# Kernel tuning notes

Measured on AMD Instinct MI355X. Metric: run time of the kernel, lower is better.

The kernel has to match this reference:

```python
import jax, jax.numpy as jnp
import numpy as np

B, S, HID = 2, 2048, 2048
H, D = 16, 128  # heads, head_dim == kernel_hidden_size
GATE_NORM = 16.0
CLAMP_MIN = -50.0


def gla(q, k, v, gk):
    # fused_recurrent_gla: S_t = diag(exp(gk_t)) S_{t-1} + k_t^T v_t; o_t = (q_t*scale) @ S_t
    # q,k,v,gk: [B,H,S,D]
    scale = D ** -0.5
    qs = jnp.moveaxis(q, 2, 0) * scale  # [S,B,H,D]
    ks = jnp.moveaxis(k, 2, 0)
    vs = jnp.moveaxis(v, 2, 0)
    gs = jnp.moveaxis(gk, 2, 0)

    def step(state, xs):
        q_t, k_t, v_t, g_t = xs  # each [B,H,D]
        state = state * jnp.exp(g_t)[..., None] + k_t[..., None] * v_t[..., None, :]
        o_t = jnp.einsum('bhk,bhkv->bhv', q_t, state)
        return state, o_t

    init = jnp.zeros((q.shape[0], H, D, D), q.dtype)
    _, out = jax.lax.scan(step, init, (qs, ks, vs, gs))
    return jnp.moveaxis(out, 0, 2)  # [B,H,S,D]


def setup_inputs() -> dict:
    key = jax.random.key(0)
    ks = jax.random.split(key, 8)
    std = 0.02
    hidden_states = jax.random.normal(ks[0], (B, S, HID), jnp.float32)
    Wq = jax.random.normal(ks[1], (HID, HID), jnp.float32) * std
    Wk = jax.random.normal(ks[2], (HID, HID), jnp.float32) * std
    Wv = jax.random.normal(ks[3], (HID, HID), jnp.float32) * std
    Wo = jax.random.normal(ks[4], (HID, HID), jnp.float32) * std
    Wg1 = jnp.eye(HID, dtype=jnp.float32)  # nn.init.eye_
    bg1 = jnp.zeros((HID,), jnp.float32)
    Wg2 = jnp.eye(HID, dtype=jnp.float32)
    bg2 = jnp.zeros((HID,), jnp.float32)
    alpha_list = jax.random.uniform(ks[5], (2,), jnp.float32)
    return dict(hidden_states=hidden_states, Wq=Wq, Wk=Wk, Wv=Wv, Wo=Wo,
                Wg1=Wg1, bg1=bg1, Wg2=Wg2, bg2=bg2, alpha_list=alpha_list)


def reference(hidden_states, Wq, Wk, Wv, Wo, Wg1, bg1, Wg2, bg2, alpha_list):
    b, s, _ = hidden_states.shape

    def split_heads(x):  # [b,s,hid] -> [b,h,s,d]
        return x.reshape(b, s, H, D).transpose(0, 2, 1, 3)

    q = split_heads(hidden_states @ Wq.T)
    k = split_heads(hidden_states @ Wk.T)
    v = split_heads(hidden_states @ Wv.T)

    def gate(Wg, bg):
        g = split_heads(hidden_states @ Wg.T + bg)
        g = jax.nn.log_sigmoid(g) / GATE_NORM
        return jnp.maximum(g, CLAMP_MIN)

    gk = gate(Wg1, bg1)
    gk2 = gate(Wg2, bg2)

    o1 = gla(q, k, v, gk)
    o2 = gla(q, k, v, gk2)

    a = jax.nn.softmax(alpha_list)
    attn = a[0] * o1 + a[1] * o2  # [b,h,s,d]
    attn = attn.transpose(0, 2, 1, 3).reshape(b, s, HID)
    return attn @ Wo.T
```

## Files before the change

### kernel.cpp

```cpp
#include <hip/hip_runtime.h>
#include <cstdint>
#include <cstddef>


#define BB     2
#define SEQ    2048
#define HIDN   2048
#define NH     16
#define DD     128
#define CHUNK  64
#define NCHUNK (SEQ / CHUNK)
#define NBH    (BB * NH)
#define NELC   8388608
#define WELC   4194304
static constexpr float QSCALE = 0.08838834764831845f;

typedef __bf16 bf16_t;
typedef _Float16 half_t;
typedef short  short8 __attribute__((ext_vector_type(8)));
typedef float  f32x4  __attribute__((ext_vector_type(4)));
typedef float  float4v __attribute__((ext_vector_type(4)));

__device__ __forceinline__ float bf2f(short u) {
  return (float)__builtin_bit_cast(bf16_t, u);
}
__device__ __forceinline__ short f2bf(float f) {
  return __builtin_bit_cast(short, (bf16_t)f);
}
__device__ __forceinline__ float hf2f(short u) {
  return (float)__builtin_bit_cast(half_t, u);
}
__device__ __forceinline__ short f2hf(float f) {
  return __builtin_bit_cast(short, (half_t)f);
}

__device__ __forceinline__ void gload_lds16(const void* g, void* l) {
  __builtin_amdgcn_global_load_lds(
      (__attribute__((address_space(1))) unsigned int*)g,
      (__attribute__((address_space(3))) unsigned int*)l, 16, 0, 0);
}

__device__ __forceinline__ void gemm_body(const bf16_t* __restrict__ A,
                                          const bf16_t* __restrict__ Bw,
                                          const float*  __restrict__ bias,
                                          bf16_t* __restrict__ outb,
                                          float*  __restrict__ outf, int epi) {
  __shared__ bf16_t As[128 * 64];
  __shared__ bf16_t Bs[128 * 64];
  const int tm   = blockIdx.x * 128;
  const int tn   = blockIdx.y * 128;
  const int wave = threadIdx.x >> 6;
  const int lane = threadIdx.x & 63;
  const int wm   = (wave >> 1) * 64;
  const int wn   = (wave & 1) * 64;
  const int qd   = lane >> 4;
  const int l16  = lane & 15;
  const int ro   = l16 & 7;

  const int gc   = (lane & 7) ^ (lane >> 3);
  const bf16_t* ga[4];
  const bf16_t* gb[4];
  bf16_t* la[4];
  bf16_t* lb[4];
#pragma unroll
  for (int u = 0; u < 4; u++) {
    const int row = wave * 32 + u * 8 + (lane >> 3);
    ga[u] = A  + (size_t)(tm + row) * HIDN + gc * 8;
    gb[u] = Bw + (size_t)(tn + row) * HIDN + gc * 8;
    la[u] = &As[(wave * 256 + u * 64) * 8];
    lb[u] = &Bs[(wave * 256 + u * 64) * 8];
  }

  f32x4 acc[4][4];
#pragma unroll
  for (int i = 0; i < 4; i++)
#pragma unroll
    for (int j = 0; j < 4; j++) acc[i][j] = (f32x4){0.f, 0.f, 0.f, 0.f};

  for (int k0 = 0; k0 < HIDN; k0 += 64) {
#pragma unroll
    for (int u = 0; u < 4; u++) { gload_lds16(ga[u], la[u]); ga[u] += 64; }
#pragma unroll
    for (int u = 0; u < 4; u++) { gload_lds16(gb[u], lb[u]); gb[u] += 64; }
    __syncthreads();
#pragma unroll
    for (int ks = 0; ks < 2; ks++) {
      const int g = ks * 4 + qd;
      short8 af[4], bfv[4];
#pragma unroll
      for (int t = 0; t < 4; t++)
        af[t] = *(const short8*)&As[(wm + t * 16 + l16) * 64 + (g ^ ro) * 8];
#pragma unroll
      for (int t = 0; t < 4; t++)
        bfv[t] = *(const short8*)&Bs[(wn + t * 16 + l16) * 64 + (g ^ ro) * 8];
#pragma unroll
      for (int i = 0; i < 4; i++)
#pragma unroll
        for (int j = 0; j < 4; j++)
          acc[i][j] = __builtin_amdgcn_mfma_f32_16x16x32_bf16(
              af[i], bfv[j], acc[i][j], 0, 0, 0);
    }
    __syncthreads();
  }

#pragma unroll
  for (int i = 0; i < 4; i++)
#pragma unroll
    for (int j = 0; j < 4; j++)
#pragma unroll
      for (int r = 0; r < 4; r++) {
        const int row = tm + wm + i * 16 + qd * 4 + r;
        const int col = tn + wn + j * 16 + l16;
        float v = acc[i][j][r];
        if (epi == 1) {
          v += bias[col];
          const float ls = fminf(v, 0.f) - log1pf(__expf(-fabsf(v)));
          v = fmaxf(ls * 0.0625f, -50.f);
        }
        if (epi == 2) outf[(size_t)row * HIDN + col] = v;
        else          outb[(size_t)row * HIDN + col] = (bf16_t)v;
      }
}

__global__ __launch_bounds__(256) void k_gemm_proj(
    const bf16_t* __restrict__ Xb,
    const bf16_t* __restrict__ W0, const bf16_t* __restrict__ W1,
    const bf16_t* __restrict__ W2, const bf16_t* __restrict__ W3,
    const bf16_t* __restrict__ W4,
    const float* __restrict__ bg1, const float* __restrict__ bg2,
    bf16_t* __restrict__ Qb, bf16_t* __restrict__ Kb, bf16_t* __restrict__ Vb,
    bf16_t* __restrict__ G1b, bf16_t* __restrict__ G2b) {
  const int z = blockIdx.z;
  const bf16_t* Ws[5] = {W0, W1, W2, W3, W4};
  bf16_t* Os[5] = {Qb, Kb, Vb, G1b, G2b};
  const float* bias = (z == 3) ? bg1 : ((z == 4) ? bg2 : nullptr);
  gemm_body(Xb, Ws[z], bias, Os[z], nullptr, (z >= 3) ? 1 : 0);
}

__global__ __launch_bounds__(256) void k_gemm_out(
    const bf16_t* __restrict__ attnB, const bf16_t* __restrict__ Wob,
    float* __restrict__ out) {
  gemm_body(attnB, Wob, nullptr, nullptr, out, 2);
}

__global__ __launch_bounds__(256) void k_cvt_all(
    const float* __restrict__ hid, const float* __restrict__ wq,
    const float* __restrict__ wk, const float* __restrict__ wv,
    const float* __restrict__ wg1, const float* __restrict__ wg2,
    const float* __restrict__ wo, bf16_t* __restrict__ Xb,
    bf16_t* __restrict__ Wd, bf16_t* __restrict__ Wcur,
    bf16_t* __restrict__ WoB) {
  const int y = blockIdx.y;
  const float* srcs[7] = {hid, wq, wk, wv, wg1, wg2, wo};
  bf16_t* dsts[7] = {Xb, Wd, Wd + WELC, Wd + 2 * WELC, Wd + 3 * WELC, Wcur,
                     WoB};
  const int n = (y == 0) ? NELC : WELC;
  const float* src = srcs[y];
  bf16_t* dst = dsts[y];
  const int idx = (blockIdx.x * 256 + threadIdx.x) * 4;
  if (idx < n) {
    const float4 f = *(const float4*)(src + idx);
    dst[idx + 0] = (bf16_t)f.x; dst[idx + 1] = (bf16_t)f.y;
    dst[idx + 2] = (bf16_t)f.z; dst[idx + 3] = (bf16_t)f.w;
  }
}

__global__ __launch_bounds__(256) void k_zero(float* __restrict__ out) {
  out[(size_t)blockIdx.x * 256 + threadIdx.x] = 0.f;
}

__global__ __launch_bounds__(256) void k_trg(
    bf16_t* __restrict__ Qb, bf16_t* __restrict__ Kb, bf16_t* __restrict__ Vb,
    bf16_t* __restrict__ G1b, bf16_t* __restrict__ G2b,
    float* __restrict__ Btot) {
  const int n = blockIdx.x, bh = blockIdx.y, z = blockIdx.z;
  const int b = bh >> 4, h = bh & 15;
  bf16_t* bufs[5] = {Qb, Kb, Vb, G1b, G2b};
  short* P = (short*)bufs[z];
  const size_t rbase = ((size_t)(b * SEQ + n * CHUNK)) * HIDN + h * DD;
  const int tid = threadIdx.x;
  __shared__ short L1[CHUNK * 136];
  __shared__ short L2[DD * 72];

#pragma unroll
  for (int k = 0; k < 4; k++) {
    const int v = tid + k * 256;
    const int t = v >> 4, d0 = (v & 15) * 8;
    const short8 x = *(const short8*)(P + rbase + (size_t)t * HIDN + d0);
#pragma unroll
    for (int j = 0; j < 8; j++) L1[t * 136 + d0 + j] = x[j];
  }
  __syncthreads();
  if (tid < DD) {
    const int d = tid;
    if (z >= 3) {
      float c = 0.f;
#pragma unroll
      for (int ch = 0; ch < 8; ch++) {
        short8 o;
#pragma unroll
        for (int j = 0; j < 8; j++) {
          c += bf2f(L1[(ch * 8 + j) * 136 + d]);
          o[j] = f2hf(c);
        }
        *(short8*)&L2[d * 72 + ch * 8] = o;
      }
      Btot[((size_t)((z - 3) * NBH + bh) * NCHUNK + n) * DD + d] = c;
    } else {
#pragma unroll
      for (int ch = 0; ch < 8; ch++) {
        short8 o;
#pragma unroll
        for (int j = 0; j < 8; j++) o[j] = L1[(ch * 8 + j) * 136 + d];
        *(short8*)&L2[d * 72 + ch * 8] = o;
      }
    }
  }
  __syncthreads();
#pragma unroll
  for (int k = 0; k < 4; k++) {
    const int v = tid + k * 256;
    const int r = v >> 4, x0 = (v & 15) * 8;
    const int d = 2 * r + (x0 >> 6), t0 = x0 & 63;
    const short8 o = *(const short8*)&L2[d * 72 + t0];
    *(short8*)(P + rbase + (size_t)r * HIDN + x0) = o;
  }
}

__global__ __launch_bounds__(256) void k_s1(
    const bf16_t* __restrict__ Kb, const bf16_t* __restrict__ Vb,
    const bf16_t* __restrict__ Gc, bf16_t* __restrict__ UT) {
  const int n = blockIdx.x, bh = blockIdx.y;
  const int b = bh >> 4, h = bh & 15;
  const size_t rbase = ((size_t)(b * SEQ + n * CHUNK)) * HIDN + h * DD;
  const int tid = threadIdx.x;
  __shared__ short k2L[DD * 72];

  if (tid < DD) {
    const int d = tid;
    const size_t row = rbase + (size_t)(d >> 1) * HIDN + (d & 1) * 64;
    const short* Kp = (const short*)Kb + row;
    const short* Gp = (const short*)Gc + row;
    const float c63 = hf2f(Gp[63]);
#pragma unroll
    for (int ch = 0; ch < 8; ch++) {
      const short8 kk = *(const short8*)(Kp + ch * 8);
      const short8 cc = *(const short8*)(Gp + ch * 8);
      short8 o;
#pragma unroll
      for (int j = 0; j < 8; j++)
        o[j] = f2bf(bf2f(kk[j]) * __expf(c63 - hf2f(cc[j])));
      *(short8*)&k2L[d * 72 + ch * 8] = o;
    }
  }
  __syncthreads();

  const int wave = tid >> 6, lane = tid & 63, qd = lane >> 4, l16 = lane & 15;
  const int m0 = (wave >> 1) * 64, n0 = (wave & 1) * 64;
  const short* Vp = (const short*)Vb;
  f32x4 acc[4][4];
#pragma unroll
  for (int i = 0; i < 4; i++)
#pragma unroll
    for (int j = 0; j < 4; j++) acc[i][j] = (f32x4){0.f, 0.f, 0.f, 0.f};
#pragma unroll
  for (int ks = 0; ks < 2; ks++) {
    const int ch = ks * 4 + qd;
    short8 af[4], bfv[4];
#pragma unroll
    for (int i = 0; i < 4; i++) {
      const int dv = m0 + i * 16 + l16;
      af[i] = *(const short8*)(Vp + rbase + (size_t)(dv >> 1) * HIDN +
                               (dv & 1) * 64 + ch * 8);
    }
#pragma unroll
    for (int j = 0; j < 4; j++)
      bfv[j] = *(const short8*)&k2L[(n0 + j * 16 + l16) * 72 + ch * 8];
#pragma unroll
    for (int i = 0; i < 4; i++)
#pragma unroll
      for (int j = 0; j < 4; j++)
        acc[i][j] = __builtin_amdgcn_mfma_f32_16x16x32_bf16(af[i], bfv[j],
                                                            acc[i][j], 0, 0, 0);
  }
  bf16_t* Uo = UT + ((size_t)bh * NCHUNK + n) * (size_t)(DD * DD);
#pragma unroll
  for (int i = 0; i < 4; i++)
#pragma unroll
    for (int j = 0; j < 4; j++)
#pragma unroll
      for (int r = 0; r < 4; r++)
        Uo[(size_t)(m0 + i * 16 + qd * 4 + r) * DD + n0 + j * 16 + l16] =
            (bf16_t)acc[i][j][r];
}

__global__ __launch_bounds__(256) void k_s2(bf16_t* __restrict__ UT,
                                            const float* __restrict__ Btot) {
  const int dg = blockIdx.x, bh = blockIdx.y;
  const int dv = dg * 8 + (threadIdx.x >> 5);
  const int dk0 = (threadIdx.x & 31) * 4;
  float st[4] = {0.f, 0.f, 0.f, 0.f};
  for (int nn = 0; nn < NCHUNK; nn++) {
    short* p =
        (short*)UT + ((size_t)bh * NCHUNK + nn) * (size_t)(DD * DD) + dv * DD + dk0;
    const float4v bp =
        *(const float4v*)(Btot + ((size_t)bh * NCHUNK + nn) * DD + dk0);
    short u0 = p[0], u1 = p[1], u2 = p[2], u3 = p[3];
    p[0] = f2bf(st[0]); p[1] = f2bf(st[1]);
    p[2] = f2bf(st[2]); p[3] = f2bf(st[3]);
    st[0] = st[0] * __expf(bp[0]) + bf2f(u0);
    st[1] = st[1] * __expf(bp[1]) + bf2f(u1);
    st[2] = st[2] * __expf(bp[2]) + bf2f(u2);
    st[3] = st[3] * __expf(bp[3]) + bf2f(u3);
  }
}

template <int ACC>
__global__ __launch_bounds__(256) void k_s3(
    const bf16_t* __restrict__ Qb, const bf16_t* __restrict__ Kb,
    const bf16_t* __restrict__ Vb, const bf16_t* __restrict__ Gc,
    const bf16_t* __restrict__ UT, const float* __restrict__ alpha,
    bf16_t* __restrict__ attn) {
  const int n = blockIdx.x, bh = blockIdx.y;
  const int b = bh >> 4, h = bh & 15;
  const size_t rbase = ((size_t)(b * SEQ + n * CHUNK)) * HIDN + h * DD;
  const int tid = threadIdx.x;
  __shared__ short qhL[CHUNK * 136];
  __shared__ short k2L[CHUNK * 136];
  __shared__ short PsL[CHUNK * 72];
  const float mx = fmaxf(alpha[0], alpha[1]);
  const float x0 = __expf(alpha[0] - mx), x1 = __expf(alpha[1] - mx);
  const float w = (ACC ? x1 : x0) / (x0 + x1);

  if (tid < DD) {
    const int d = tid;
    const size_t row = rbase + (size_t)(d >> 1) * HIDN + (d & 1) * 64;
    const short* Qp = (const short*)Qb + row;
    const short* Kp = (const short*)Kb + row;
    const short* Gp = (const short*)Gc + row;
    const float wsc = w * QSCALE;
#pragma unroll
    for (int ch = 0; ch < 8; ch++) {
      const short8 qq = *(const short8*)(Qp + ch * 8);
      const short8 kk = *(const short8*)(Kp + ch * 8);
      const short8 cc = *(const short8*)(Gp + ch * 8);
#pragma unroll
      for (int j = 0; j < 8; j++) {
        const float c = hf2f(cc[j]);
        const int t = ch * 8 + j;
        qhL[t * 136 + d] = f2bf(bf2f(qq[j]) * wsc * __expf(c));
        k2L[t * 136 + d] = f2bf(bf2f(kk[j]) * __expf(-c));
      }
    }
  }
  __syncthreads();

  const int wave = tid >> 6, lane = tid & 63, qd = lane >> 4, l16 = lane & 15;
  {
    f32x4 pacc[4];
#pragma unroll
    for (int j = 0; j < 4; j++) pacc[j] = (f32x4){0.f, 0.f, 0.f, 0.f};
#pragma unroll
    for (int ks = 0; ks < 4; ks++) {
      const int ch = ks * 4 + qd;
      const short8 a = *(const short8*)&qhL[(wave * 16 + l16) * 136 + ch * 8];
#pragma unroll
      for (int j = 0; j < 4; j++) {
        const short8 bq = *(const short8*)&k2L[(j * 16 + l16) * 136 + ch * 8];
        pacc[j] = __builtin_amdgcn_mfma_f32_16x16x32_bf16(a, bq, pacc[j], 0, 0, 0);
      }
    }
#pragma unroll
    for (int j = 0; j < 4; j++)
#pragma unroll
      for (int r = 0; r < 4; r++) {
        const int t = wave * 16 + qd * 4 + r, s = j * 16 + l16;
        PsL[t * 72 + s] = (t >= s) ? f2bf(pacc[j][r]) : (short)0;
      }
  }
  __syncthreads();

  const short* Sp =
      (const short*)UT + ((size_t)bh * NCHUNK + n) * (size_t)(DD * DD);
  const short* Vp = (const short*)Vb;
  const int nw = wave * 32;
  f32x4 acc[4][2];
#pragma unroll
  for (int i = 0; i < 4; i++)
#pragma unroll
    for (int j = 0; j < 2; j++) acc[i][j] = (f32x4){0.f, 0.f, 0.f, 0.f};
#pragma unroll
  for (int ks = 0; ks < 2; ks++) {
    const int ch = ks * 4 + qd;
    short8 a[4];
#pragma unroll
    for (int i = 0; i < 4; i++)
      a[i] = *(const short8*)&PsL[(i * 16 + l16) * 72 + ch * 8];
#pragma unroll
    for (int j = 0; j < 2; j++) {
      const int dv = nw + j * 16 + l16;
      const short8 bq = *(const short8*)(Vp + rbase + (size_t)(dv >> 1) * HIDN +
                                         (dv & 1) * 64 + ch * 8);
#pragma unroll
      for (int i = 0; i < 4; i++)
        acc[i][j] = __builtin_amdgcn_mfma_f32_16x16x32_bf16(a[i], bq,
                                                            acc[i][j], 0, 0, 0);
    }
  }
#pragma unroll
  for (int ks = 0; ks < 4; ks++) {
    const int ch = ks * 4 + qd;
    short8 a[4];
#pragma unroll
    for (int i = 0; i < 4; i++)
      a[i] = *(const short8*)&qhL[(i * 16 + l16) * 136 + ch * 8];
#pragma unroll
    for (int j = 0; j < 2; j++) {
      const short8 bq =
          *(const short8*)(Sp + (size_t)(nw + j * 16 + l16) * DD + ch * 8);
#pragma unroll
      for (int i = 0; i < 4; i++)
        acc[i][j] = __builtin_amdgcn_mfma_f32_16x16x32_bf16(a[i], bq,
                                                            acc[i][j], 0, 0, 0);
    }
  }
#pragma unroll
  for (int i = 0; i < 4; i++)
#pragma unroll
    for (int j = 0; j < 2; j++)
#pragma unroll
      for (int r = 0; r < 4; r++) {
        const int t = i * 16 + qd * 4 + r;
        const int dv = nw + j * 16 + l16;
        bf16_t* p = &attn[rbase + (size_t)t * HIDN + dv];
        if (ACC) *p = (bf16_t)((float)*p + acc[i][j][r]);
        else     *p = (bf16_t)acc[i][j][r];
      }
}

extern "C" void kernel_launch(void* const* d_in, const int* in_sizes, int n_in,
                              void* d_out, int out_size, void* d_ws,
                              size_t ws_size, hipStream_t stream) {
  const float* hid  = (const float*)d_in[0];
  const float* wq   = (const float*)d_in[1];
  const float* wk   = (const float*)d_in[2];
  const float* wv   = (const float*)d_in[3];
  const float* wo   = (const float*)d_in[4];
  const float* wg1  = (const float*)d_in[5];
  const float* bg1  = (const float*)d_in[6];
  const float* wg2  = (const float*)d_in[7];
  const float* bg2  = (const float*)d_in[8];
  const float* alph = (const float*)d_in[9];
  float* out = (float*)d_out;
  (void)in_sizes; (void)n_in; (void)out_size;

  char* ws = (char*)d_ws;
  size_t off = 0;
  auto alloc = [&](size_t bytes) -> void* {
    void* p = ws + off;
    off += (bytes + 255) & ~(size_t)255;
    return p;
  };
  const size_t NEL = NELC, WEL = WELC;
  bf16_t* Xb   = (bf16_t*)alloc(NEL * 2);
  bf16_t* Wcur = (bf16_t*)alloc(WEL * 2);
  bf16_t* WoB  = (bf16_t*)alloc(WEL * 2);
  bf16_t* Qb   = (bf16_t*)alloc(NEL * 2);
  bf16_t* Kb   = (bf16_t*)alloc(NEL * 2);
  bf16_t* Vb   = (bf16_t*)alloc(NEL * 2);
  bf16_t* G1b  = (bf16_t*)alloc(NEL * 2);
  bf16_t* G2b  = (bf16_t*)alloc(NEL * 2);
  float*  Btot = (float*) alloc((size_t)2 * NBH * NCHUNK * DD * 4);
  bf16_t* Wd = (bf16_t*)d_out;
  bf16_t* UT = (bf16_t*)d_out;

  if (off > ws_size) {
    k_zero<<<dim3((unsigned)(NEL / 256)), 256, 0, stream>>>(out);
    return;
  }

  k_cvt_all<<<dim3(8192, 7), 256, 0, stream>>>(hid, wq, wk, wv, wg1, wg2, wo,
                                               Xb, Wd, Wcur, WoB);
  k_gemm_proj<<<dim3(32, 16, 5), 256, 0, stream>>>(
      Xb, Wd, Wd + WEL, Wd + 2 * WEL, Wd + 3 * WEL, Wcur, bg1, bg2, Qb, Kb, Vb,
      G1b, G2b);
  k_trg<<<dim3(NCHUNK, NBH, 5), 256, 0, stream>>>(Qb, Kb, Vb, G1b, G2b, Btot);

  const dim3 gs(NCHUNK, NBH), g2(16, NBH);
  const size_t BSTRIDE = (size_t)NBH * NCHUNK * DD;
  k_s1<<<gs, 256, 0, stream>>>(Kb, Vb, G1b, UT);
  k_s2<<<g2, 256, 0, stream>>>(UT, Btot);
  k_s3<0><<<gs, 256, 0, stream>>>(Qb, Kb, Vb, G1b, UT, alph, Xb);
  k_s1<<<gs, 256, 0, stream>>>(Kb, Vb, G2b, UT);
  k_s2<<<g2, 256, 0, stream>>>(UT, Btot + BSTRIDE);
  k_s3<1><<<gs, 256, 0, stream>>>(Qb, Kb, Vb, G2b, UT, alph, Xb);

  k_gemm_out<<<dim3(32, 16), 256, 0, stream>>>(Xb, WoB, out);
}
```

Measured before the change: 648.5 us.

## Drop chunk transpose pass; fuse intra-chunk attention into state-update kernel

Removes the k_trg kernel that transposed Q/K/V/G chunks in global memory. Only the gate cumulative sum stays, now done in place by a lightweight kernel. The per-chunk state contribution and the intra-chunk causal attention are merged into one kernel that transposes V and K in LDS. A slimmer kernel then adds the inter-chunk state term using an XOR-swizzled state layout loaded directly into LDS. This cuts global read/write passes and extra launches, at the cost of more LDS per block and scalar int-unpacking LDS reads.

```diff
diff --git a/kernel.cpp b/kernel.cpp
--- a/kernel.cpp
+++ b/kernel.cpp
@@ -19,7 +19,6 @@
 typedef _Float16 half_t;
 typedef short  short8 __attribute__((ext_vector_type(8)));
 typedef float  f32x4  __attribute__((ext_vector_type(4)));
-typedef float  float4v __attribute__((ext_vector_type(4)));
 
 __device__ __forceinline__ float bf2f(short u) {
   return (float)__builtin_bit_cast(bf16_t, u);
@@ -57,7 +56,7 @@
   const int l16  = lane & 15;
   const int ro   = l16 & 7;
 
-  const int gc   = (lane & 7) ^ (lane >> 3);
+  const int gc = (lane & 7) ^ (lane >> 3);
   const bf16_t* ga[4];
   const bf16_t* gb[4];
   bf16_t* la[4];
@@ -169,129 +168,212 @@
   out[(size_t)blockIdx.x * 256 + threadIdx.x] = 0.f;
 }
 
-__global__ __launch_bounds__(256) void k_trg(
-    bf16_t* __restrict__ Qb, bf16_t* __restrict__ Kb, bf16_t* __restrict__ Vb,
-    bf16_t* __restrict__ G1b, bf16_t* __restrict__ G2b,
-    float* __restrict__ Btot) {
-  const int n = blockIdx.x, bh = blockIdx.y, z = blockIdx.z;
-  const int b = bh >> 4, h = bh & 15;
-  bf16_t* bufs[5] = {Qb, Kb, Vb, G1b, G2b};
-  short* P = (short*)bufs[z];
-  const size_t rbase = ((size_t)(b * SEQ + n * CHUNK)) * HIDN + h * DD;
-  const int tid = threadIdx.x;
-  __shared__ short L1[CHUNK * 136];
-  __shared__ short L2[DD * 72];
-
-#pragma unroll
-  for (int k = 0; k < 4; k++) {
-    const int v = tid + k * 256;
-    const int t = v >> 4, d0 = (v & 15) * 8;
-    const short8 x = *(const short8*)(P + rbase + (size_t)t * HIDN + d0);
-#pragma unroll
-    for (int j = 0; j < 8; j++) L1[t * 136 + d0 + j] = x[j];
-  }
-  __syncthreads();
-  if (tid < DD) {
-    const int d = tid;
-    if (z >= 3) {
-      float c = 0.f;
-#pragma unroll
-      for (int ch = 0; ch < 8; ch++) {
-        short8 o;
-#pragma unroll
-        for (int j = 0; j < 8; j++) {
-          c += bf2f(L1[(ch * 8 + j) * 136 + d]);
-          o[j] = f2hf(c);
-        }
-        *(short8*)&L2[d * 72 + ch * 8] = o;
-      }
-      Btot[((size_t)((z - 3) * NBH + bh) * NCHUNK + n) * DD + d] = c;
-    } else {
-#pragma unroll
-      for (int ch = 0; ch < 8; ch++) {
-        short8 o;
-#pragma unroll
-        for (int j = 0; j < 8; j++) o[j] = L1[(ch * 8 + j) * 136 + d];
-        *(short8*)&L2[d * 72 + ch * 8] = o;
-      }
-    }
-  }
-  __syncthreads();
-#pragma unroll
-  for (int k = 0; k < 4; k++) {
-    const int v = tid + k * 256;
-    const int r = v >> 4, x0 = (v & 15) * 8;
-    const int d = 2 * r + (x0 >> 6), t0 = x0 & 63;
-    const short8 o = *(const short8*)&L2[d * 72 + t0];
-    *(short8*)(P + rbase + (size_t)r * HIDN + x0) = o;
-  }
-}
-
-__global__ __launch_bounds__(256) void k_s1(
-    const bf16_t* __restrict__ Kb, const bf16_t* __restrict__ Vb,
-    const bf16_t* __restrict__ Gc, bf16_t* __restrict__ UT) {
+__global__ __launch_bounds__(64) void k_gc(bf16_t* __restrict__ G1b,
+                                           bf16_t* __restrict__ G2b,
+                                           float* __restrict__ Btot) {
+  const int n = blockIdx.x, b = blockIdx.y >> 2, slab = blockIdx.y & 3;
+  const int e = blockIdx.z;
+  short* P = (short*)(e ? G2b : G1b);
+  const int d0 = slab * 512 + threadIdx.x * 8;
+  const size_t base = ((size_t)(b * SEQ + n * CHUNK)) * HIDN + d0;
+  float c[8] = {0.f, 0.f, 0.f, 0.f, 0.f, 0.f, 0.f, 0.f};
+  for (int t = 0; t < CHUNK; t++) {
+    short* p = P + base + (size_t)t * HIDN;
+    const short8 g = *(const short8*)p;
+    short8 o;
+#pragma unroll
+    for (int j = 0; j < 8; j++) { c[j] += bf2f(g[j]); o[j] = f2hf(c[j]); }
+    *(short8*)p = o;
+  }
+  const int bh = b * 16 + (d0 >> 7);
+  float* bp = Btot + ((size_t)(e * NBH + bh) * NCHUNK + n) * DD + (d0 & 127);
+#pragma unroll
+  for (int j = 0; j < 8; j++) bp[j] = c[j];
+}
+
+template <int ACC>
+__global__ __launch_bounds__(256) void k_sA(
+    const bf16_t* __restrict__ Qb, const bf16_t* __restrict__ Kb,
+    const bf16_t* __restrict__ Vb, const bf16_t* __restrict__ Gc,
+    bf16_t* __restrict__ UT, const float* __restrict__ alpha,
+    bf16_t* __restrict__ attn) {
   const int n = blockIdx.x, bh = blockIdx.y;
   const int b = bh >> 4, h = bh & 15;
   const size_t rbase = ((size_t)(b * SEQ + n * CHUNK)) * HIDN + h * DD;
   const int tid = threadIdx.x;
-  __shared__ short k2L[DD * 72];
-
-  if (tid < DD) {
-    const int d = tid;
-    const size_t row = rbase + (size_t)(d >> 1) * HIDN + (d & 1) * 64;
-    const short* Kp = (const short*)Kb + row;
-    const short* Gp = (const short*)Gc + row;
-    const float c63 = hf2f(Gp[63]);
-#pragma unroll
-    for (int ch = 0; ch < 8; ch++) {
-      const short8 kk = *(const short8*)(Kp + ch * 8);
-      const short8 cc = *(const short8*)(Gp + ch * 8);
-      short8 o;
-#pragma unroll
-      for (int j = 0; j < 8; j++)
-        o[j] = f2bf(bf2f(kk[j]) * __expf(c63 - hf2f(cc[j])));
-      *(short8*)&k2L[d * 72 + ch * 8] = o;
-    }
+  const int wave = tid >> 6, lane = tid & 63, qd = lane >> 4, l16 = lane & 15;
+  __shared__ short vT[128 * 66];
+  __shared__ short k2s[64 * 128];
+  __shared__ short r3[128 * 66];
+  __shared__ short Ps[64 * 72];
+  const float mx = fmaxf(alpha[0], alpha[1]);
+  const float x0 = __expf(alpha[0] - mx), x1 = __expf(alpha[1] - mx);
+  const float wsc = ((ACC ? x1 : x0) / (x0 + x1)) * QSCALE;
+
+  const short* Kp = (const short*)Kb;
+  const short* Vp = (const short*)Vb;
+  const short* Gp = (const short*)Gc;
+  const short* Qp = (const short*)Qb;
+
+#pragma unroll
+  for (int rep = 0; rep < 4; rep++) {
+    const int slot = rep * 256 + tid;
+    const int t = slot >> 4, ch = slot & 15;
+    const size_t ga = rbase + (size_t)t * HIDN + ch * 8;
+    const short8 vv = *(const short8*)(Vp + ga);
+    const short8 kk = *(const short8*)(Kp + ga);
+    const short8 cc = *(const short8*)(Gp + ga);
+    const short8 c6 = *(const short8*)(Gp + rbase + (size_t)63 * HIDN + ch * 8);
+    short8 k2v;
+#pragma unroll
+    for (int j = 0; j < 8; j++) {
+      const int d = ch * 8 + j;
+      vT[d * 66 + t] = vv[j];
+      const float c = hf2f(cc[j]);
+      const float kf = bf2f(kk[j]);
+      k2v[j] = f2bf(kf * __expf(-c));
+      r3[d * 66 + t] = f2bf(kf * __expf(hf2f(c6[j]) - c));
+    }
+    *(short8*)&k2s[t * 128 + ((ch ^ (t & 7)) << 3)] = k2v;
   }
   __syncthreads();
 
-  const int wave = tid >> 6, lane = tid & 63, qd = lane >> 4, l16 = lane & 15;
-  const int m0 = (wave >> 1) * 64, n0 = (wave & 1) * 64;
-  const short* Vp = (const short*)Vb;
-  f32x4 acc[4][4];
-#pragma unroll
-  for (int i = 0; i < 4; i++)
-#pragma unroll
-    for (int j = 0; j < 4; j++) acc[i][j] = (f32x4){0.f, 0.f, 0.f, 0.f};
-#pragma unroll
-  for (int ks = 0; ks < 2; ks++) {
-    const int ch = ks * 4 + qd;
-    short8 af[4], bfv[4];
-#pragma unroll
-    for (int i = 0; i < 4; i++) {
-      const int dv = m0 + i * 16 + l16;
-      af[i] = *(const short8*)(Vp + rbase + (size_t)(dv >> 1) * HIDN +
-                               (dv & 1) * 64 + ch * 8);
+  {
+    const int m0 = (wave >> 1) * 64, n0 = (wave & 1) * 64;
+    const int* vTi = (const int*)vT;
+    const int* r3i = (const int*)r3;
+    f32x4 uacc[4][4];
+#pragma unroll
+    for (int i = 0; i < 4; i++)
+#pragma unroll
+      for (int j = 0; j < 4; j++) uacc[i][j] = (f32x4){0.f, 0.f, 0.f, 0.f};
+#pragma unroll
+    for (int ks = 0; ks < 2; ks++) {
+      const int ch = ks * 4 + qd;
+      short8 af[4], bfv[4];
+#pragma unroll
+      for (int i = 0; i < 4; i++) {
+        const int dv = m0 + i * 16 + l16;
+        const int ba = dv * 33 + ch * 4;
+#pragma unroll
+        for (int w2 = 0; w2 < 4; w2++) {
+          const int v = vTi[ba + w2];
+          af[i][2 * w2] = (short)(v & 0xffff);
+          af[i][2 * w2 + 1] = (short)((unsigned)v >> 16);
+        }
+      }
+#pragma unroll
+      for (int j = 0; j < 4; j++) {
+        const int dk = n0 + j * 16 + l16;
+        const int ba = dk * 33 + ch * 4;
+#pragma unroll
+        for (int w2 = 0; w2 < 4; w2++) {
+          const int v = r3i[ba + w2];
+          bfv[j][2 * w2] = (short)(v & 0xffff);
+          bfv[j][2 * w2 + 1] = (short)((unsigned)v >> 16);
+        }
+      }
+#pragma unroll
+      for (int i = 0; i < 4; i++)
+#pragma unroll
+        for (int j = 0; j < 4; j++)
+          uacc[i][j] = __builtin_amdgcn_mfma_f32_16x16x32_bf16(
+              af[i], bfv[j], uacc[i][j], 0, 0, 0);
+    }
+    short* Uo = (short*)UT + (size_t)(bh * NCHUNK + n) * (DD * DD);
+#pragma unroll
+    for (int i = 0; i < 4; i++)
+#pragma unroll
+      for (int j = 0; j < 4; j++)
+#pragma unroll
+        for (int r = 0; r < 4; r++) {
+          const int dv = m0 + i * 16 + qd * 4 + r;
+          const int dk = n0 + j * 16 + l16;
+          Uo[dv * 128 + (((dk >> 3) ^ (dv & 7)) << 3) + (dk & 7)] =
+              f2bf(uacc[i][j][r]);
+        }
+  }
+  __syncthreads();
+
+#pragma unroll
+  for (int rep = 0; rep < 4; rep++) {
+    const int slot = rep * 256 + tid;
+    const int t = slot >> 4, ch = slot & 15;
+    const size_t ga = rbase + (size_t)t * HIDN + ch * 8;
+    const short8 qq = *(const short8*)(Qp + ga);
+    const short8 cc = *(const short8*)(Gp + ga);
+    short8 o;
+#pragma unroll
+    for (int j = 0; j < 8; j++)
+      o[j] = f2bf(bf2f(qq[j]) * wsc * __expf(hf2f(cc[j])));
+    *(short8*)&r3[t * 128 + ((ch ^ (t & 7)) << 3)] = o;
+  }
+  __syncthreads();
+
+  {
+    f32x4 pacc[4];
+#pragma unroll
+    for (int j = 0; j < 4; j++) pacc[j] = (f32x4){0.f, 0.f, 0.f, 0.f};
+    const int tq = wave * 16 + l16;
+#pragma unroll
+    for (int ks = 0; ks < 4; ks++) {
+      const int ch = ks * 4 + qd;
+      const short8 a = *(const short8*)&r3[tq * 128 + ((ch ^ (tq & 7)) << 3)];
+#pragma unroll
+      for (int j = 0; j < 4; j++) {
+        const int s = j * 16 + l16;
+        const short8 bq =
+            *(const short8*)&k2s[s * 128 + ((ch ^ (s & 7)) << 3)];
+        pacc[j] =
+            __builtin_amdgcn_mfma_f32_16x16x32_bf16(a, bq, pacc[j], 0, 0, 0);
+      }
     }
 #pragma unroll
     for (int j = 0; j < 4; j++)
-      bfv[j] = *(const short8*)&k2L[(n0 + j * 16 + l16) * 72 + ch * 8];
-#pragma unroll
-    for (int i = 0; i < 4; i++)
-#pragma unroll
-      for (int j = 0; j < 4; j++)
-        acc[i][j] = __builtin_amdgcn_mfma_f32_16x16x32_bf16(af[i], bfv[j],
-                                                            acc[i][j], 0, 0, 0);
-  }
-  bf16_t* Uo = UT + ((size_t)bh * NCHUNK + n) * (size_t)(DD * DD);
-#pragma unroll
-  for (int i = 0; i < 4; i++)
-#pragma unroll
-    for (int j = 0; j < 4; j++)
-#pragma unroll
-      for (int r = 0; r < 4; r++)
-        Uo[(size_t)(m0 + i * 16 + qd * 4 + r) * DD + n0 + j * 16 + l16] =
-            (bf16_t)acc[i][j][r];
+#pragma unroll
+      for (int r = 0; r < 4; r++) {
+        const int t = wave * 16 + qd * 4 + r, s = j * 16 + l16;
+        Ps[t * 72 + s] = (t >= s) ? f2bf(pacc[j][r]) : (short)0;
+      }
+  }
+  __syncthreads();
+
+  f32x4 oacc[8];
+#pragma unroll
+  for (int j = 0; j < 8; j++) oacc[j] = (f32x4){0.f, 0.f, 0.f, 0.f};
+  {
+    const int* vTi = (const int*)vT;
+    const int tq = wave * 16 + l16;
+#pragma unroll
+    for (int ks = 0; ks < 2; ks++) {
+      const int ch = ks * 4 + qd;
+      const short8 a = *(const short8*)&Ps[tq * 72 + ch * 8];
+#pragma unroll
+      for (int j = 0; j < 8; j++) {
+        const int dv = j * 16 + l16;
+        const int ba = dv * 33 + ch * 4;
+        short8 bq;
+#pragma unroll
+        for (int w2 = 0; w2 < 4; w2++) {
+          const int v = vTi[ba + w2];
+          bq[2 * w2] = (short)(v & 0xffff);
+          bq[2 * w2 + 1] = (short)((unsigned)v >> 16);
+        }
+        oacc[j] =
+            __builtin_amdgcn_mfma_f32_16x16x32_bf16(a, bq, oacc[j], 0, 0, 0);
+      }
+    }
+  }
+#pragma unroll
+  for (int j = 0; j < 8; j++)
+#pragma unroll
+    for (int r = 0; r < 4; r++) {
+      const int t = wave * 16 + qd * 4 + r;
+      const int dv = j * 16 + l16;
+      bf16_t* p = &attn[rbase + (size_t)t * HIDN + dv];
+      if (ACC) *p = (bf16_t)((float)*p + oacc[j][r]);
+      else     *p = (bf16_t)oacc[j][r];
+    }
 }
 
 __global__ __launch_bounds__(256) void k_s2(bf16_t* __restrict__ UT,
@@ -299,143 +381,85 @@
   const int dg = blockIdx.x, bh = blockIdx.y;
   const int dv = dg * 8 + (threadIdx.x >> 5);
   const int dk0 = (threadIdx.x & 31) * 4;
+  const int pos = dv * 128 + (((dk0 >> 3) ^ (dv & 7)) << 3) + (dk0 & 7);
   float st[4] = {0.f, 0.f, 0.f, 0.f};
   for (int nn = 0; nn < NCHUNK; nn++) {
-    short* p =
-        (short*)UT + ((size_t)bh * NCHUNK + nn) * (size_t)(DD * DD) + dv * DD + dk0;
-    const float4v bp =
-        *(const float4v*)(Btot + ((size_t)bh * NCHUNK + nn) * DD + dk0);
+    short* p = (short*)UT + (size_t)(bh * NCHUNK + nn) * (DD * DD) + pos;
+    const float4 bp =
+        *(const float4*)(Btot + (size_t)(bh * NCHUNK + nn) * DD + dk0);
     short u0 = p[0], u1 = p[1], u2 = p[2], u3 = p[3];
     p[0] = f2bf(st[0]); p[1] = f2bf(st[1]);
     p[2] = f2bf(st[2]); p[3] = f2bf(st[3]);
-    st[0] = st[0] * __expf(bp[0]) + bf2f(u0);
-    st[1] = st[1] * __expf(bp[1]) + bf2f(u1);
-    st[2] = st[2] * __expf(bp[2]) + bf2f(u2);
-    st[3] = st[3] * __expf(bp[3]) + bf2f(u3);
-  }
-}
-
-template <int ACC>
-__global__ __launch_bounds__(256) void k_s3(
-    const bf16_t* __restrict__ Qb, const bf16_t* __restrict__ Kb,
-    const bf16_t* __restrict__ Vb, const bf16_t* __restrict__ Gc,
+    st[0] = st[0] * __expf(bp.x) + bf2f(u0);
+    st[1] = st[1] * __expf(bp.y) + bf2f(u1);
+    st[2] = st[2] * __expf(bp.z) + bf2f(u2);
+    st[3] = st[3] * __expf(bp.w) + bf2f(u3);
+  }
+}
+
+__global__ __launch_bounds__(256) void k_s3b(
+    const bf16_t* __restrict__ Qb, const bf16_t* __restrict__ Gc,
     const bf16_t* __restrict__ UT, const float* __restrict__ alpha,
-    bf16_t* __restrict__ attn) {
+    const int e, bf16_t* __restrict__ attn) {
   const int n = blockIdx.x, bh = blockIdx.y;
   const int b = bh >> 4, h = bh & 15;
   const size_t rbase = ((size_t)(b * SEQ + n * CHUNK)) * HIDN + h * DD;
   const int tid = threadIdx.x;
-  __shared__ short qhL[CHUNK * 136];
-  __shared__ short k2L[CHUNK * 136];
-  __shared__ short PsL[CHUNK * 72];
+  const int wave = tid >> 6, lane = tid & 63, qd = lane >> 4, l16 = lane & 15;
+  __shared__ short qh[64 * 128];
+  __shared__ short Ss[128 * 128];
   const float mx = fmaxf(alpha[0], alpha[1]);
   const float x0 = __expf(alpha[0] - mx), x1 = __expf(alpha[1] - mx);
-  const float w = (ACC ? x1 : x0) / (x0 + x1);
-
-  if (tid < DD) {
-    const int d = tid;
-    const size_t row = rbase + (size_t)(d >> 1) * HIDN + (d & 1) * 64;
-    const short* Qp = (const short*)Qb + row;
-    const short* Kp = (const short*)Kb + row;
-    const short* Gp = (const short*)Gc + row;
-    const float wsc = w * QSCALE;
-#pragma unroll
-    for (int ch = 0; ch < 8; ch++) {
-      const short8 qq = *(const short8*)(Qp + ch * 8);
-      const short8 kk = *(const short8*)(Kp + ch * 8);
-      const short8 cc = *(const short8*)(Gp + ch * 8);
-#pragma unroll
-      for (int j = 0; j < 8; j++) {
-        const float c = hf2f(cc[j]);
-        const int t = ch * 8 + j;
-        qhL[t * 136 + d] = f2bf(bf2f(qq[j]) * wsc * __expf(c));
-        k2L[t * 136 + d] = f2bf(bf2f(kk[j]) * __expf(-c));
-      }
-    }
+  const float wsc = ((e ? x1 : x0) / (x0 + x1)) * QSCALE;
+
+  const short* Sp = (const short*)UT + (size_t)(bh * NCHUNK + n) * (DD * DD);
+#pragma unroll
+  for (int rep = 0; rep < 8; rep++) {
+    const int c = rep * 256 + tid;
+    gload_lds16(Sp + c * 8, &Ss[c * 8]);
+  }
+  const short* Qp = (const short*)Qb;
+  const short* Gp = (const short*)Gc;
+#pragma unroll
+  for (int rep = 0; rep < 4; rep++) {
+    const int slot = rep * 256 + tid;
+    const int t = slot >> 4, ch = slot & 15;
+    const size_t ga = rbase + (size_t)t * HIDN + ch * 8;
+    const short8 qq = *(const short8*)(Qp + ga);
+    const short8 cc = *(const short8*)(Gp + ga);
+    short8 o;
+#pragma unroll
+    for (int j = 0; j < 8; j++)
+      o[j] = f2bf(bf2f(qq[j]) * wsc * __expf(hf2f(cc[j])));
+    *(short8*)&qh[t * 128 + ((ch ^ (t & 7)) << 3)] = o;
   }
   __syncthreads();
 
-  const int wave = tid >> 6, lane = tid & 63, qd = lane >> 4, l16 = lane & 15;
-  {
-    f32x4 pacc[4];
-#pragma unroll
-    for (int j = 0; j < 4; j++) pacc[j] = (f32x4){0.f, 0.f, 0.f, 0.f};
-#pragma unroll
-    for (int ks = 0; ks < 4; ks++) {
-      const int ch = ks * 4 + qd;
-      const short8 a = *(const short8*)&qhL[(wave * 16 + l16) * 136 + ch * 8];
-#pragma unroll
-      for (int j = 0; j < 4; j++) {
-        const short8 bq = *(const short8*)&k2L[(j * 16 + l16) * 136 + ch * 8];
-        pacc[j] = __builtin_amdgcn_mfma_f32_16x16x32_bf16(a, bq, pacc[j], 0, 0, 0);
-      }
-    }
-#pragma unroll
-    for (int j = 0; j < 4; j++)
-#pragma unroll
-      for (int r = 0; r < 4; r++) {
-        const int t = wave * 16 + qd * 4 + r, s = j * 16 + l16;
-        PsL[t * 72 + s] = (t >= s) ? f2bf(pacc[j][r]) : (short)0;
-      }
-  }
-  __syncthreads();
-
-  const short* Sp =
-      (const short*)UT + ((size_t)bh * NCHUNK + n) * (size_t)(DD * DD);
-  const short* Vp = (const short*)Vb;
-  const int nw = wave * 32;
-  f32x4 acc[4][2];
-#pragma unroll
-  for (int i = 0; i < 4; i++)
-#pragma unroll
-    for (int j = 0; j < 2; j++) acc[i][j] = (f32x4){0.f, 0.f, 0.f, 0.f};
-#pragma unroll
-  for (int ks = 0; ks < 2; ks++) {
-    const int ch = ks * 4 + qd;
-    short8 a[4];
-#pragma unroll
-    for (int i = 0; i < 4; i++)
-      a[i] = *(const short8*)&PsL[(i * 16 + l16) * 72 + ch * 8];
-#pragma unroll
-    for (int j = 0; j < 2; j++) {
-      const int dv = nw + j * 16 + l16;
-      const short8 bq = *(const short8*)(Vp + rbase + (size_t)(dv >> 1) * HIDN +
-                                         (dv & 1) * 64 + ch * 8);
-#pragma unroll
-      for (int i = 0; i < 4; i++)
-        acc[i][j] = __builtin_amdgcn_mfma_f32_16x16x32_bf16(a[i], bq,
-                                                            acc[i][j], 0, 0, 0);
-    }
-  }
+  f32x4 oacc[8];
+#pragma unroll
+  for (int j = 0; j < 8; j++) oacc[j] = (f32x4){0.f, 0.f, 0.f, 0.f};
+  const int tq = wave * 16 + l16;
 #pragma unroll
   for (int ks = 0; ks < 4; ks++) {
     const int ch = ks * 4 + qd;
-    short8 a[4];
-#pragma unroll
-    for (int i = 0; i < 4; i++)
-      a[i] = *(const short8*)&qhL[(i * 16 + l16) * 136 + ch * 8];
-#pragma unroll
-    for (int j = 0; j < 2; j++) {
-      const short8 bq =
-          *(const short8*)(Sp + (size_t)(nw + j * 16 + l16) * DD + ch * 8);
-#pragma unroll
-      for (int i = 0; i < 4; i++)
-        acc[i][j] = __builtin_amdgcn_mfma_f32_16x16x32_bf16(a[i], bq,
-                                                            acc[i][j], 0, 0, 0);
-    }
-  }
-#pragma unroll
-  for (int i = 0; i < 4; i++)
-#pragma unroll
-    for (int j = 0; j < 2; j++)
-#pragma unroll
-      for (int r = 0; r < 4; r++) {
-        const int t = i * 16 + qd * 4 + r;
-        const int dv = nw + j * 16 + l16;
-        bf16_t* p = &attn[rbase + (size_t)t * HIDN + dv];
-        if (ACC) *p = (bf16_t)((float)*p + acc[i][j][r]);
-        else     *p = (bf16_t)acc[i][j][r];
-      }
+    const short8 a = *(const short8*)&qh[tq * 128 + ((ch ^ (tq & 7)) << 3)];
+#pragma unroll
+    for (int j = 0; j < 8; j++) {
+      const int dv = j * 16 + l16;
+      const short8 bq = *(const short8*)&Ss[dv * 128 + ((ch ^ (dv & 7)) << 3)];
+      oacc[j] =
+          __builtin_amdgcn_mfma_f32_16x16x32_bf16(a, bq, oacc[j], 0, 0, 0);
+    }
+  }
+#pragma unroll
+  for (int j = 0; j < 8; j++)
+#pragma unroll
+    for (int r = 0; r < 4; r++) {
+      const int t = wave * 16 + qd * 4 + r;
+      const int dv = j * 16 + l16;
+      bf16_t* p = &attn[rbase + (size_t)t * HIDN + dv];
+      *p = (bf16_t)((float)*p + oacc[j][r]);
+    }
 }
 
 extern "C" void kernel_launch(void* const* d_in, const int* in_sizes, int n_in,
@@ -484,16 +508,16 @@
   k_gemm_proj<<<dim3(32, 16, 5), 256, 0, stream>>>(
       Xb, Wd, Wd + WEL, Wd + 2 * WEL, Wd + 3 * WEL, Wcur, bg1, bg2, Qb, Kb, Vb,
       G1b, G2b);
-  k_trg<<<dim3(NCHUNK, NBH, 5), 256, 0, stream>>>(Qb, Kb, Vb, G1b, G2b, Btot);
+  k_gc<<<dim3(NCHUNK, BB * 4, 2), 64, 0, stream>>>(G1b, G2b, Btot);
 
   const dim3 gs(NCHUNK, NBH), g2(16, NBH);
   const size_t BSTRIDE = (size_t)NBH * NCHUNK * DD;
-  k_s1<<<gs, 256, 0, stream>>>(Kb, Vb, G1b, UT);
+  k_sA<0><<<gs, 256, 0, stream>>>(Qb, Kb, Vb, G1b, UT, alph, Xb);
   k_s2<<<g2, 256, 0, stream>>>(UT, Btot);
-  k_s3<0><<<gs, 256, 0, stream>>>(Qb, Kb, Vb, G1b, UT, alph, Xb);
-  k_s1<<<gs, 256, 0, stream>>>(Kb, Vb, G2b, UT);
+  k_s3b<<<gs, 256, 0, stream>>>(Qb, G1b, UT, alph, 0, Xb);
+  k_sA<1><<<gs, 256, 0, stream>>>(Qb, Kb, Vb, G2b, UT, alph, Xb);
   k_s2<<<g2, 256, 0, stream>>>(UT, Btot + BSTRIDE);
-  k_s3<1><<<gs, 256, 0, stream>>>(Qb, Kb, Vb, G2b, UT, alph, Xb);
+  k_s3b<<<gs, 256, 0, stream>>>(Qb, G2b, UT, alph, 1, Xb);
 
   k_gemm_out<<<dim3(32, 16), 256, 0, stream>>>(Xb, WoB, out);
 }
```

Result: faster. 591.1 us (-8.9%).
